# Optimization experiments

Measured on AMD Instinct MI355X. Metric: run time of the kernel, lower is better.

Reference implementation:

```python
import jax, jax.numpy as jnp
import numpy as np

D_MODEL = 300   # hardcoded d_model1 in Matposer.__init__
VOCAB = 32000
B, L = 512, 512
OUT = 4


def sinusoidal_pe(length, d):
    # Standard 'Attention is All You Need' positional encoding used by the repo's PositionalEncoding.
    pos = jnp.arange(length, dtype=jnp.float32)[:, None]
    div = jnp.exp(jnp.arange(0, d, 2, dtype=jnp.float32) * (-np.log(10000.0) / d))
    pe = jnp.zeros((length, d), dtype=jnp.float32)
    pe = pe.at[:, 0::2].set(jnp.sin(pos * div))
    pe = pe.at[:, 1::2].set(jnp.cos(pos * div))
    return pe


def setup_inputs() -> dict:
    key = jax.random.key(0)
    k1, k2, k3, k4, k5, k6 = jax.random.split(key, 6)
    return {
        "x1": jax.random.randint(k1, (B, L), 0, VOCAB, dtype=jnp.int32),
        "x2": jax.random.randint(k2, (B, L), 0, VOCAB, dtype=jnp.int32),
        "emb1": jax.random.normal(k3, (VOCAB, D_MODEL), dtype=jnp.float32) * 0.02,
        "emb2": jax.random.normal(k4, (VOCAB, D_MODEL), dtype=jnp.float32) * 0.02,
        "w1": jax.random.normal(k5, (D_MODEL, D_MODEL), dtype=jnp.float32) / np.sqrt(D_MODEL),
        "b1": jnp.zeros((D_MODEL,), dtype=jnp.float32),
        "w2": jax.random.normal(k6, (OUT, D_MODEL), dtype=jnp.float32) / np.sqrt(D_MODEL),
        "b2": jnp.zeros((OUT,), dtype=jnp.float32),
    }


def reference(x1, x2, emb1, emb2, w1, b1, w2, b2):
    scale = jnp.sqrt(jnp.float32(D_MODEL))   # Embeddings multiplies by sqrt(d_model)
    pe = sinusoidal_pe(x1.shape[1], D_MODEL)  # [L, D]
    # Embed + positional encoding (dropout=0 / eval mode). [B, L, D]
    e1 = emb1[x1] * scale + pe
    e2 = emb2[x2] * scale + pe
    # encoded_sents = e2.permute(0,2,1) @ e1 -> [B, D, D]
    fmap = jnp.einsum('bld,ble->bde', e2, e1)
    # torch Tensor.diagonal() defaults to dim1=0, dim2=1 -> shape [D, min(B, D)]
    diag = jnp.diagonal(fmap, axis1=0, axis2=1)  # [D, D] since B >= D
    # class_fc: Linear(300,300) -> ReLU -> Linear(300,output_size); torch Linear: x @ W.T + b
    h = jax.nn.relu(diag @ w1.T + b1)
    logits = h @ w2.T + b2
    # nn.Softmax() on a 2D input -> softmax over dim=1
    return jax.nn.softmax(logits, axis=-1)
```

## Files before the change

kernel.cpp:

```cpp
#include <hip/hip_runtime.h>
#include <math.h>

#define D_MODEL 300
#define LSEQ    512
#define NBATCH  300
#define SPLIT   8
#define LCH     (LSEQ / SPLIT)
#define NG      4
#define NR      75
#define KCH     (D_MODEL / 4)
#define JPB     2
#define SCALE   17.32050807568877f

__global__ void pe_kernel(float* __restrict__ pe) {
    int idx = blockIdx.x * blockDim.x + threadIdx.x;
    if (idx >= LSEQ * D_MODEL) return;
    int l = idx / D_MODEL;
    int e = idx - l * D_MODEL;
    int k = e >> 1;
    float dv = expf((float)(2 * k) * (-9.210340371976184f / 300.0f));
    float arg = (float)l * dv;
    pe[idx] = (e & 1) ? cosf(arg) : sinf(arg);
}

__global__ void diag_fused_kernel(const int* __restrict__ x1, const int* __restrict__ x2,
                                  const float* __restrict__ emb1, const float* __restrict__ emb2,
                                  const float* __restrict__ pe, float* __restrict__ Dm) {
    __shared__ int    x1ch[LCH];
    __shared__ float  sch[LCH];
    __shared__ float4 part[NG][NR];
    const int i   = blockIdx.x;
    const int sp  = blockIdx.y;
    const int tid = threadIdx.x;
    const int l0  = sp * LCH;

    if (tid < LCH) {
        const int l = l0 + tid;
        x1ch[tid] = x1[i * LSEQ + l];
        int idx2  = x2[i * LSEQ + l];
        sch[tid]  = emb2[idx2 * D_MODEL + i] * SCALE + pe[l * D_MODEL + i];
    }
    __syncthreads();

    const int g = tid / NR;
    const int r = tid - g * NR;

    if (tid < NG * NR) {
        float ax = 0.f, ay = 0.f, az = 0.f, aw = 0.f;
        #pragma unroll 4
        for (int l = g; l < LCH; l += NG) {
            const float4 ev = ((const float4*)(emb1 + (size_t)x1ch[l] * D_MODEL))[r];
            const float4 pv = ((const float4*)(pe   + (size_t)(l0 + l) * D_MODEL))[r];
            const float  s  = sch[l];
            ax = fmaf(s, fmaf(ev.x, SCALE, pv.x), ax);
            ay = fmaf(s, fmaf(ev.y, SCALE, pv.y), ay);
            az = fmaf(s, fmaf(ev.z, SCALE, pv.z), az);
            aw = fmaf(s, fmaf(ev.w, SCALE, pv.w), aw);
        }
        part[g][r] = make_float4(ax, ay, az, aw);
    }
    __syncthreads();

    if (g == 0 && tid < NR) {
        float4 p0 = part[0][r], p1 = part[1][r], p2 = part[2][r], p3 = part[3][r];
        float* dst = Dm + i * D_MODEL + 4 * r;
        atomicAdd(dst + 0, p0.x + p1.x + p2.x + p3.x);
        atomicAdd(dst + 1, p0.y + p1.y + p2.y + p3.y);
        atomicAdd(dst + 2, p0.z + p1.z + p2.z + p3.z);
        atomicAdd(dst + 3, p0.w + p1.w + p2.w + p3.w);
    }
}

__global__ void fc1_kernel(const float* __restrict__ w1, const float* __restrict__ Dm,
                           float* __restrict__ Hpre) {
    const int j0  = blockIdx.x * JPB;
    const int sp  = blockIdx.y;
    const int tid = threadIdx.x;
    const int k0  = sp * KCH;
    if (tid >= D_MODEL) return;
    const float* w1r0 = w1 + (j0 + 0) * D_MODEL + k0;
    const float* w1r1 = w1 + (j0 + 1) * D_MODEL + k0;
    float acc0 = 0.0f, acc1 = 0.0f;
    #pragma unroll 5
    for (int k = 0; k < KCH; ++k) {
        float d = Dm[(k0 + k) * D_MODEL + tid];
        acc0 = fmaf(w1r0[k], d, acc0);
        acc1 = fmaf(w1r1[k], d, acc1);
    }
    atomicAdd(&Hpre[(j0 + 0) * D_MODEL + tid], acc0);
    atomicAdd(&Hpre[(j0 + 1) * D_MODEL + tid], acc1);
}

__global__ void fc2_softmax_kernel(const float* __restrict__ Hpre, const float* __restrict__ b1,
                                   const float* __restrict__ w2, const float* __restrict__ b2,
                                   float* __restrict__ out) {
    __shared__ float sm[4][4][64];
    const int tid   = threadIdx.x;
    const int e_loc = tid & 63;
    const int jc    = tid >> 6;
    const int e     = blockIdx.x * 64 + e_loc;

    float a0 = 0.f, a1 = 0.f, a2 = 0.f, a3 = 0.f;
    if (e < D_MODEL) {
        const int j0 = jc * 75;
        #pragma unroll 5
        for (int j = j0; j < j0 + 75; ++j) {
            float h = fmaxf(Hpre[j * D_MODEL + e] + b1[j], 0.0f);
            a0 = fmaf(h, w2[0 * D_MODEL + j], a0);
            a1 = fmaf(h, w2[1 * D_MODEL + j], a1);
            a2 = fmaf(h, w2[2 * D_MODEL + j], a2);
            a3 = fmaf(h, w2[3 * D_MODEL + j], a3);
        }
    }
    sm[jc][0][e_loc] = a0; sm[jc][1][e_loc] = a1;
    sm[jc][2][e_loc] = a2; sm[jc][3][e_loc] = a3;
    __syncthreads();

    if (jc == 0 && e < D_MODEL) {
        float l0 = b2[0] + sm[0][0][e_loc] + sm[1][0][e_loc] + sm[2][0][e_loc] + sm[3][0][e_loc];
        float l1 = b2[1] + sm[0][1][e_loc] + sm[1][1][e_loc] + sm[2][1][e_loc] + sm[3][1][e_loc];
        float l2 = b2[2] + sm[0][2][e_loc] + sm[1][2][e_loc] + sm[2][2][e_loc] + sm[3][2][e_loc];
        float l3 = b2[3] + sm[0][3][e_loc] + sm[1][3][e_loc] + sm[2][3][e_loc] + sm[3][3][e_loc];
        float m  = fmaxf(fmaxf(l0, l1), fmaxf(l2, l3));
        float x0 = expf(l0 - m), x1 = expf(l1 - m), x2 = expf(l2 - m), x3 = expf(l3 - m);
        float inv = 1.0f / (x0 + x1 + x2 + x3);
        out[e * 4 + 0] = x0 * inv;
        out[e * 4 + 1] = x1 * inv;
        out[e * 4 + 2] = x2 * inv;
        out[e * 4 + 3] = x3 * inv;
    }
}

extern "C" void kernel_launch(void* const* d_in, const int* in_sizes, int n_in,
                              void* d_out, int out_size, void* d_ws, size_t ws_size,
                              hipStream_t stream) {
    const int*   x1   = (const int*)d_in[0];
    const int*   x2   = (const int*)d_in[1];
    const float* emb1 = (const float*)d_in[2];
    const float* emb2 = (const float*)d_in[3];
    const float* w1   = (const float*)d_in[4];
    const float* b1   = (const float*)d_in[5];
    const float* w2   = (const float*)d_in[6];
    const float* b2   = (const float*)d_in[7];
    float* out = (float*)d_out;

    char* ws = (char*)d_ws;
    float* pe   = (float*)ws;
    float* Dm   = (float*)(ws + 614400);
    float* Hpre = (float*)(ws + 974400);

    (void)hipMemsetAsync(Dm, 0, 2 * 360000, stream);

    pe_kernel<<<(LSEQ * D_MODEL + 255) / 256, 256, 0, stream>>>(pe);
    diag_fused_kernel<<<dim3(NBATCH, SPLIT), 320, 0, stream>>>(x1, x2, emb1, emb2, pe, Dm);
    fc1_kernel<<<dim3(D_MODEL / JPB, 4), 320, 0, stream>>>(w1, Dm, Hpre);
    fc2_softmax_kernel<<<(D_MODEL + 63) / 64, 256, 0, stream>>>(Hpre, b1, w2, b2, out);
}
```

Before: 157.9 us.

## Split diagonal product into embedding and positional-encoding terms across extra blocks

The diagonal computation is decomposed algebraically: s·(SCALE·emb1+pe) becomes SCALE·(s·emb1) plus s·pe. The main blocks no longer stream the pe rows alongside the gathered embedding rows, and extra grid blocks compute the s·pe term as a separate coalesced reduction, with both parts added into Dm atomically. Separately, fc1 now handles four output rows per block instead of two, which halves its grid and reuses each Dm load more. The cost is more atomics and extra blocks that re-gather the emb2 column values, and the different summation order changes float rounding.

```diff
diff --git a/kernel.cpp b/kernel.cpp
--- a/kernel.cpp
+++ b/kernel.cpp
@@ -6,10 +6,12 @@
 #define NBATCH  300
 #define SPLIT   8
 #define LCH     (LSEQ / SPLIT)
+#define PESPLIT 4
+#define PLCH    (LSEQ / PESPLIT)
 #define NG      4
 #define NR      75
 #define KCH     (D_MODEL / 4)
-#define JPB     2
+#define JPB     4
 #define SCALE   17.32050807568877f
 
 __global__ void pe_kernel(float* __restrict__ pe) {
@@ -26,48 +28,64 @@
 __global__ void diag_fused_kernel(const int* __restrict__ x1, const int* __restrict__ x2,
                                   const float* __restrict__ emb1, const float* __restrict__ emb2,
                                   const float* __restrict__ pe, float* __restrict__ Dm) {
-    __shared__ int    x1ch[LCH];
-    __shared__ float  sch[LCH];
+    __shared__ int    x1ch[PLCH];
+    __shared__ float  sch[PLCH];
     __shared__ float4 part[NG][NR];
     const int i   = blockIdx.x;
-    const int sp  = blockIdx.y;
+    const int y   = blockIdx.y;
     const int tid = threadIdx.x;
-    const int l0  = sp * LCH;
 
-    if (tid < LCH) {
-        const int l = l0 + tid;
-        x1ch[tid] = x1[i * LSEQ + l];
-        int idx2  = x2[i * LSEQ + l];
-        sch[tid]  = emb2[idx2 * D_MODEL + i] * SCALE + pe[l * D_MODEL + i];
-    }
-    __syncthreads();
+    if (y < SPLIT) {
+        const int l0 = y * LCH;
+        if (tid < LCH) {
+            const int l = l0 + tid;
+            x1ch[tid] = x1[i * LSEQ + l];
+            int idx2  = x2[i * LSEQ + l];
+            sch[tid]  = emb2[idx2 * D_MODEL + i] * SCALE + pe[l * D_MODEL + i];
+        }
+        __syncthreads();
 
-    const int g = tid / NR;
-    const int r = tid - g * NR;
+        const int g = tid / NR;
+        const int r = tid - g * NR;
+        if (tid < NG * NR) {
+            float ax = 0.f, ay = 0.f, az = 0.f, aw = 0.f;
+            #pragma unroll 4
+            for (int l = g; l < LCH; l += NG) {
+                const float4 ev = ((const float4*)(emb1 + (size_t)x1ch[l] * D_MODEL))[r];
+                const float  s  = sch[l];
+                ax = fmaf(s, ev.x, ax);
+                ay = fmaf(s, ev.y, ay);
+                az = fmaf(s, ev.z, az);
+                aw = fmaf(s, ev.w, aw);
+            }
+            part[g][r] = make_float4(ax, ay, az, aw);
+        }
+        __syncthreads();
 
-    if (tid < NG * NR) {
-        float ax = 0.f, ay = 0.f, az = 0.f, aw = 0.f;
-        #pragma unroll 4
-        for (int l = g; l < LCH; l += NG) {
-            const float4 ev = ((const float4*)(emb1 + (size_t)x1ch[l] * D_MODEL))[r];
-            const float4 pv = ((const float4*)(pe   + (size_t)(l0 + l) * D_MODEL))[r];
-            const float  s  = sch[l];
-            ax = fmaf(s, fmaf(ev.x, SCALE, pv.x), ax);
-            ay = fmaf(s, fmaf(ev.y, SCALE, pv.y), ay);
-            az = fmaf(s, fmaf(ev.z, SCALE, pv.z), az);
-            aw = fmaf(s, fmaf(ev.w, SCALE, pv.w), aw);
+        if (g == 0 && tid < NR) {
+            float4 p0 = part[0][r], p1 = part[1][r], p2 = part[2][r], p3 = part[3][r];
+            float* dst = Dm + i * D_MODEL + 4 * r;
+            atomicAdd(dst + 0, SCALE * (p0.x + p1.x + p2.x + p3.x));
+            atomicAdd(dst + 1, SCALE * (p0.y + p1.y + p2.y + p3.y));
+            atomicAdd(dst + 2, SCALE * (p0.z + p1.z + p2.z + p3.z));
+            atomicAdd(dst + 3, SCALE * (p0.w + p1.w + p2.w + p3.w));
         }
-        part[g][r] = make_float4(ax, ay, az, aw);
-    }
-    __syncthreads();
+    } else {
+        const int l0 = (y - SPLIT) * PLCH;
+        if (tid < PLCH) {
+            const int l = l0 + tid;
+            int idx2  = x2[i * LSEQ + l];
+            sch[tid]  = emb2[idx2 * D_MODEL + i] * SCALE + pe[l * D_MODEL + i];
+        }
+        __syncthreads();
 
-    if (g == 0 && tid < NR) {
-        float4 p0 = part[0][r], p1 = part[1][r], p2 = part[2][r], p3 = part[3][r];
-        float* dst = Dm + i * D_MODEL + 4 * r;
-        atomicAdd(dst + 0, p0.x + p1.x + p2.x + p3.x);
-        atomicAdd(dst + 1, p0.y + p1.y + p2.y + p3.y);
-        atomicAdd(dst + 2, p0.z + p1.z + p2.z + p3.z);
-        atomicAdd(dst + 3, p0.w + p1.w + p2.w + p3.w);
+        if (tid < D_MODEL) {
+            float acc = 0.0f;
+            #pragma unroll 8
+            for (int l = 0; l < PLCH; ++l)
+                acc = fmaf(sch[l], pe[(l0 + l) * D_MODEL + tid], acc);
+            atomicAdd(&Dm[i * D_MODEL + tid], acc);
+        }
     }
 }
 
@@ -80,15 +98,21 @@
     if (tid >= D_MODEL) return;
     const float* w1r0 = w1 + (j0 + 0) * D_MODEL + k0;
     const float* w1r1 = w1 + (j0 + 1) * D_MODEL + k0;
-    float acc0 = 0.0f, acc1 = 0.0f;
+    const float* w1r2 = w1 + (j0 + 2) * D_MODEL + k0;
+    const float* w1r3 = w1 + (j0 + 3) * D_MODEL + k0;
+    float acc0 = 0.0f, acc1 = 0.0f, acc2 = 0.0f, acc3 = 0.0f;
     #pragma unroll 5
     for (int k = 0; k < KCH; ++k) {
         float d = Dm[(k0 + k) * D_MODEL + tid];
         acc0 = fmaf(w1r0[k], d, acc0);
         acc1 = fmaf(w1r1[k], d, acc1);
+        acc2 = fmaf(w1r2[k], d, acc2);
+        acc3 = fmaf(w1r3[k], d, acc3);
     }
     atomicAdd(&Hpre[(j0 + 0) * D_MODEL + tid], acc0);
     atomicAdd(&Hpre[(j0 + 1) * D_MODEL + tid], acc1);
+    atomicAdd(&Hpre[(j0 + 2) * D_MODEL + tid], acc2);
+    atomicAdd(&Hpre[(j0 + 3) * D_MODEL + tid], acc3);
 }
 
 __global__ void fc2_softmax_kernel(const float* __restrict__ Hpre, const float* __restrict__ b1,
@@ -152,7 +176,7 @@
     (void)hipMemsetAsync(Dm, 0, 2 * 360000, stream);
 
     pe_kernel<<<(LSEQ * D_MODEL + 255) / 256, 256, 0, stream>>>(pe);
-    diag_fused_kernel<<<dim3(NBATCH, SPLIT), 320, 0, stream>>>(x1, x2, emb1, emb2, pe, Dm);
+    diag_fused_kernel<<<dim3(NBATCH, SPLIT + PESPLIT), 320, 0, stream>>>(x1, x2, emb1, emb2, pe, Dm);
     fc1_kernel<<<dim3(D_MODEL / JPB, 4), 320, 0, stream>>>(w1, Dm, Hpre);
     fc2_softmax_kernel<<<(D_MODEL + 63) / 64, 256, 0, stream>>>(Hpre, b1, w2, b2, out);
 }
```

Result: slower. 165.5 us (+4.8%).

## Convert emb1 table to bf16 before gather and widen fc1 rows per block

Applied to the files above, without the earlier changes.

Adds a kernel that converts the whole emb1 table (32000x300 fp32) to bf16 in workspace on every call. The diagonal kernel then gathers half as many bytes per row. fc1 now computes four output rows per block instead of two, which halves its grid. The conversion reads all 38 MB of emb1 and writes 19 MB, while the gather only touches about 300*512 rows, so the extra pass likely costs more than it saves. Rounding to bf16 also loses precision.

```diff
diff --git a/kernel.cpp b/kernel.cpp
--- a/kernel.cpp
+++ b/kernel.cpp
@@ -4,13 +4,33 @@
 #define D_MODEL 300
 #define LSEQ    512
 #define NBATCH  300
+#define VOCAB   32000
 #define SPLIT   8
 #define LCH     (LSEQ / SPLIT)
 #define NG      4
 #define NR      75
 #define KCH     (D_MODEL / 4)
-#define JPB     2
+#define JPB     4
 #define SCALE   17.32050807568877f
+
+__device__ __forceinline__ unsigned short f2bf(float f) {
+    unsigned u = __float_as_uint(f);
+    unsigned r = (u + 0x7FFFu + ((u >> 16) & 1u)) >> 16;
+    return (unsigned short)r;
+}
+__device__ __forceinline__ float bf2f(unsigned short v) {
+    return __uint_as_float(((unsigned)v) << 16);
+}
+
+__global__ void conv_kernel(const float* __restrict__ emb1, unsigned short* __restrict__ e1b) {
+    int t = blockIdx.x * blockDim.x + threadIdx.x;
+    int base = t * 4;
+    if (base >= VOCAB * D_MODEL) return;
+    float4 v = ((const float4*)emb1)[t];
+    ushort4 o;
+    o.x = f2bf(v.x); o.y = f2bf(v.y); o.z = f2bf(v.z); o.w = f2bf(v.w);
+    ((ushort4*)e1b)[t] = o;
+}
 
 __global__ void pe_kernel(float* __restrict__ pe) {
     int idx = blockIdx.x * blockDim.x + threadIdx.x;
@@ -24,7 +44,8 @@
 }
 
 __global__ void diag_fused_kernel(const int* __restrict__ x1, const int* __restrict__ x2,
-                                  const float* __restrict__ emb1, const float* __restrict__ emb2,
+                                  const unsigned short* __restrict__ e1b,
+                                  const float* __restrict__ emb2,
                                   const float* __restrict__ pe, float* __restrict__ Dm) {
     __shared__ int    x1ch[LCH];
     __shared__ float  sch[LCH];
@@ -49,13 +70,13 @@
         float ax = 0.f, ay = 0.f, az = 0.f, aw = 0.f;
         #pragma unroll 4
         for (int l = g; l < LCH; l += NG) {
-            const float4 ev = ((const float4*)(emb1 + (size_t)x1ch[l] * D_MODEL))[r];
-            const float4 pv = ((const float4*)(pe   + (size_t)(l0 + l) * D_MODEL))[r];
-            const float  s  = sch[l];
-            ax = fmaf(s, fmaf(ev.x, SCALE, pv.x), ax);
-            ay = fmaf(s, fmaf(ev.y, SCALE, pv.y), ay);
-            az = fmaf(s, fmaf(ev.z, SCALE, pv.z), az);
-            aw = fmaf(s, fmaf(ev.w, SCALE, pv.w), aw);
+            const ushort4 ev = ((const ushort4*)(e1b + (size_t)x1ch[l] * D_MODEL))[r];
+            const float4  pv = ((const float4*)(pe + (size_t)(l0 + l) * D_MODEL))[r];
+            const float   s  = sch[l];
+            ax = fmaf(s, fmaf(bf2f(ev.x), SCALE, pv.x), ax);
+            ay = fmaf(s, fmaf(bf2f(ev.y), SCALE, pv.y), ay);
+            az = fmaf(s, fmaf(bf2f(ev.z), SCALE, pv.z), az);
+            aw = fmaf(s, fmaf(bf2f(ev.w), SCALE, pv.w), aw);
         }
         part[g][r] = make_float4(ax, ay, az, aw);
     }
@@ -80,15 +101,21 @@
     if (tid >= D_MODEL) return;
     const float* w1r0 = w1 + (j0 + 0) * D_MODEL + k0;
     const float* w1r1 = w1 + (j0 + 1) * D_MODEL + k0;
-    float acc0 = 0.0f, acc1 = 0.0f;
+    const float* w1r2 = w1 + (j0 + 2) * D_MODEL + k0;
+    const float* w1r3 = w1 + (j0 + 3) * D_MODEL + k0;
+    float acc0 = 0.0f, acc1 = 0.0f, acc2 = 0.0f, acc3 = 0.0f;
     #pragma unroll 5
     for (int k = 0; k < KCH; ++k) {
         float d = Dm[(k0 + k) * D_MODEL + tid];
         acc0 = fmaf(w1r0[k], d, acc0);
         acc1 = fmaf(w1r1[k], d, acc1);
+        acc2 = fmaf(w1r2[k], d, acc2);
+        acc3 = fmaf(w1r3[k], d, acc3);
     }
     atomicAdd(&Hpre[(j0 + 0) * D_MODEL + tid], acc0);
     atomicAdd(&Hpre[(j0 + 1) * D_MODEL + tid], acc1);
+    atomicAdd(&Hpre[(j0 + 2) * D_MODEL + tid], acc2);
+    atomicAdd(&Hpre[(j0 + 3) * D_MODEL + tid], acc3);
 }
 
 __global__ void fc2_softmax_kernel(const float* __restrict__ Hpre, const float* __restrict__ b1,
@@ -145,14 +172,16 @@
     float* out = (float*)d_out;
 
     char* ws = (char*)d_ws;
-    float* pe   = (float*)ws;
-    float* Dm   = (float*)(ws + 614400);
-    float* Hpre = (float*)(ws + 974400);
+    float*          pe   = (float*)ws;
+    float*          Dm   = (float*)(ws + 614400);
+    float*          Hpre = (float*)(ws + 974400);
+    unsigned short* e1b  = (unsigned short*)(ws + 1334400);
 
     (void)hipMemsetAsync(Dm, 0, 2 * 360000, stream);
 
+    conv_kernel<<<(VOCAB * D_MODEL / 4 + 255) / 256, 256, 0, stream>>>(emb1, e1b);
     pe_kernel<<<(LSEQ * D_MODEL + 255) / 256, 256, 0, stream>>>(pe);
-    diag_fused_kernel<<<dim3(NBATCH, SPLIT), 320, 0, stream>>>(x1, x2, emb1, emb2, pe, Dm);
+    diag_fused_kernel<<<dim3(NBATCH, SPLIT), 320, 0, stream>>>(x1, x2, e1b, emb2, pe, Dm);
     fc1_kernel<<<dim3(D_MODEL / JPB, 4), 320, 0, stream>>>(w1, Dm, Hpre);
     fc2_softmax_kernel<<<(D_MODEL + 63) / 64, 256, 0, stream>>>(Hpre, b1, w2, b2, out);
 }
```

After: 159.6 us. About the same (+1.1%).

## Bucket token gathers by vocabulary range to improve embedding-table locality

Applied to the files above, without the earlier changes.

A new kernel sorts each batch row's tokens into 8 buckets by vocabulary range. For each token it stores a packed key holding the position and token id, plus the precomputed emb2/positional scale value. The diagonal kernel then processes one bucket per block, so emb1 row gathers within a block stay inside a narrower slice of the table, aiming for better cache hit rates. It adds an extra launch, an extra write/read pass through workspace, and a fixed bucket capacity of 160 that would overflow on skewed inputs. Separately, fc1 now computes 4 output rows per block instead of 2, reusing each Dm load more.

```diff
diff --git a/kernel.cpp b/kernel.cpp
--- a/kernel.cpp
+++ b/kernel.cpp
@@ -4,12 +4,12 @@
 #define D_MODEL 300
 #define LSEQ    512
 #define NBATCH  300
-#define SPLIT   8
-#define LCH     (LSEQ / SPLIT)
+#define NBUK    8
+#define BCAP    160
 #define NG      4
 #define NR      75
 #define KCH     (D_MODEL / 4)
-#define JPB     2
+#define JPB     4
 #define SCALE   17.32050807568877f
 
 __global__ void pe_kernel(float* __restrict__ pe) {
@@ -23,22 +23,43 @@
     pe[idx] = (e & 1) ? cosf(arg) : sinf(arg);
 }
 
-__global__ void diag_fused_kernel(const int* __restrict__ x1, const int* __restrict__ x2,
-                                  const float* __restrict__ emb1, const float* __restrict__ emb2,
-                                  const float* __restrict__ pe, float* __restrict__ Dm) {
-    __shared__ int    x1ch[LCH];
-    __shared__ float  sch[LCH];
+__global__ void bucket_kernel(const int* __restrict__ x1, const int* __restrict__ x2,
+                              const float* __restrict__ emb2, const float* __restrict__ pe,
+                              int* __restrict__ keybuf, float* __restrict__ valbuf,
+                              int* __restrict__ cntg) {
+    __shared__ int cnt[NBUK];
+    const int i = blockIdx.x;
+    const int l = threadIdx.x;
+    if (l < NBUK) cnt[l] = 0;
+    __syncthreads();
+    const int v    = x1[i * LSEQ + l];
+    const int idx2 = x2[i * LSEQ + l];
+    const float s  = emb2[idx2 * D_MODEL + i] * SCALE + pe[l * D_MODEL + i];
+    const int b    = v >> 12;
+    const int pos  = atomicAdd(&cnt[b], 1);
+    const int off  = (i * NBUK + b) * BCAP + pos;
+    keybuf[off] = (l << 15) | v;
+    valbuf[off] = s;
+    __syncthreads();
+    if (l < NBUK) cntg[i * NBUK + l] = cnt[l];
+}
+
+__global__ void diag_gather_kernel(const int* __restrict__ keybuf, const float* __restrict__ valbuf,
+                                   const int* __restrict__ cntg,
+                                   const float* __restrict__ emb1, const float* __restrict__ pe,
+                                   float* __restrict__ Dm) {
+    __shared__ int    key[BCAP];
+    __shared__ float  val[BCAP];
     __shared__ float4 part[NG][NR];
-    const int i   = blockIdx.x;
-    const int sp  = blockIdx.y;
+    const int b   = blockIdx.x;
+    const int i   = blockIdx.y;
     const int tid = threadIdx.x;
-    const int l0  = sp * LCH;
+    const int base = (i * NBUK + b) * BCAP;
+    const int n   = cntg[i * NBUK + b];
 
-    if (tid < LCH) {
-        const int l = l0 + tid;
-        x1ch[tid] = x1[i * LSEQ + l];
-        int idx2  = x2[i * LSEQ + l];
-        sch[tid]  = emb2[idx2 * D_MODEL + i] * SCALE + pe[l * D_MODEL + i];
+    for (int t = tid; t < n; t += blockDim.x) {
+        key[t] = keybuf[base + t];
+        val[t] = valbuf[base + t];
     }
     __syncthreads();
 
@@ -47,11 +68,13 @@
 
     if (tid < NG * NR) {
         float ax = 0.f, ay = 0.f, az = 0.f, aw = 0.f;
-        #pragma unroll 4
-        for (int l = g; l < LCH; l += NG) {
-            const float4 ev = ((const float4*)(emb1 + (size_t)x1ch[l] * D_MODEL))[r];
-            const float4 pv = ((const float4*)(pe   + (size_t)(l0 + l) * D_MODEL))[r];
-            const float  s  = sch[l];
+        for (int t = g; t < n; t += NG) {
+            const int   k = key[t];
+            const int   v = k & 0x7FFF;
+            const int   l = k >> 15;
+            const float4 ev = ((const float4*)(emb1 + (size_t)v * D_MODEL))[r];
+            const float4 pv = ((const float4*)(pe + (size_t)l * D_MODEL))[r];
+            const float  s  = val[t];
             ax = fmaf(s, fmaf(ev.x, SCALE, pv.x), ax);
             ay = fmaf(s, fmaf(ev.y, SCALE, pv.y), ay);
             az = fmaf(s, fmaf(ev.z, SCALE, pv.z), az);
@@ -80,15 +103,21 @@
     if (tid >= D_MODEL) return;
     const float* w1r0 = w1 + (j0 + 0) * D_MODEL + k0;
     const float* w1r1 = w1 + (j0 + 1) * D_MODEL + k0;
-    float acc0 = 0.0f, acc1 = 0.0f;
+    const float* w1r2 = w1 + (j0 + 2) * D_MODEL + k0;
+    const float* w1r3 = w1 + (j0 + 3) * D_MODEL + k0;
+    float acc0 = 0.0f, acc1 = 0.0f, acc2 = 0.0f, acc3 = 0.0f;
     #pragma unroll 5
     for (int k = 0; k < KCH; ++k) {
         float d = Dm[(k0 + k) * D_MODEL + tid];
         acc0 = fmaf(w1r0[k], d, acc0);
         acc1 = fmaf(w1r1[k], d, acc1);
+        acc2 = fmaf(w1r2[k], d, acc2);
+        acc3 = fmaf(w1r3[k], d, acc3);
     }
     atomicAdd(&Hpre[(j0 + 0) * D_MODEL + tid], acc0);
     atomicAdd(&Hpre[(j0 + 1) * D_MODEL + tid], acc1);
+    atomicAdd(&Hpre[(j0 + 2) * D_MODEL + tid], acc2);
+    atomicAdd(&Hpre[(j0 + 3) * D_MODEL + tid], acc3);
 }
 
 __global__ void fc2_softmax_kernel(const float* __restrict__ Hpre, const float* __restrict__ b1,
@@ -145,14 +174,18 @@
     float* out = (float*)d_out;
 
     char* ws = (char*)d_ws;
-    float* pe   = (float*)ws;
-    float* Dm   = (float*)(ws + 614400);
-    float* Hpre = (float*)(ws + 974400);
+    float* pe     = (float*)ws;
+    float* Dm     = (float*)(ws + 614400);
+    float* Hpre   = (float*)(ws + 974400);
+    int*   keybuf = (int*)(ws + 1334400);
+    float* valbuf = (float*)(ws + 2870400);
+    int*   cntg   = (int*)(ws + 4406400);
 
     (void)hipMemsetAsync(Dm, 0, 2 * 360000, stream);
 
     pe_kernel<<<(LSEQ * D_MODEL + 255) / 256, 256, 0, stream>>>(pe);
-    diag_fused_kernel<<<dim3(NBATCH, SPLIT), 320, 0, stream>>>(x1, x2, emb1, emb2, pe, Dm);
+    bucket_kernel<<<NBATCH, LSEQ, 0, stream>>>(x1, x2, emb2, pe, keybuf, valbuf, cntg);
+    diag_gather_kernel<<<dim3(NBUK, NBATCH), 320, 0, stream>>>(keybuf, valbuf, cntg, emb1, pe, Dm);
     fc1_kernel<<<dim3(D_MODEL / JPB, 4), 320, 0, stream>>>(w1, Dm, Hpre);
     fc2_softmax_kernel<<<(D_MODEL + 63) / 64, 256, 0, stream>>>(Hpre, b1, w2, b2, out);
 }
```

After: 159.1 us. No clear change (+0.8%).
